# Performance work log

Hardware: AMD Instinct MI355X
Metric: run time of the kernel (lower is better)

The kernel has to match this reference:

```python
import jax, jax.numpy as jnp
import numpy as np

B, N, D, KD = 8, 2048, 64, 64

def setup_inputs() -> dict:
    key = jax.random.key(0)
    ks = jax.random.split(key, 7)
    s = 1.0 / np.sqrt(D)
    return {
        "x":  jax.random.normal(ks[0], (B, N, D), dtype=jnp.float32),
        "Wq": jax.random.normal(ks[1], (D, KD), dtype=jnp.float32) * s,
        "bq": jnp.zeros((KD,), jnp.float32),
        "Wk": jax.random.normal(ks[2], (D, KD), dtype=jnp.float32) * s,
        "bk": jnp.zeros((KD,), jnp.float32),
        "Wv": jax.random.normal(ks[3], (D, KD), dtype=jnp.float32) * s,
        "bv": jnp.zeros((KD,), jnp.float32),
    }

def reference(x, Wq, bq, Wk, bk, Wv, bv):
    # Q,K,V: [B,N,KD]
    Q = x @ Wq + bq
    K = x @ Wk + bk
    V = x @ Wv + bv
    # scores: [B,N,N] (note: original applies NO 1/sqrt(d) scaling)
    scores = jnp.einsum('bij,bkj->bik', Q, K)
    probs = jax.nn.softmax(scores, axis=-1)
    # mean-threshold sparsification: keep entries above the row mean
    mask = (probs > jnp.mean(probs, axis=-1, keepdims=True)).astype(probs.dtype)
    sparse = probs * mask
    out = jnp.einsum('bij,bjk->bik', sparse, V)  # [B,N,KD]
    return out
```

## Files before the change

kernel.cpp:

```cpp
#include <hip/hip_runtime.h>

#define NB 8
#define NS 2048
#define ND 64
#define LOG2E 1.44269504f

typedef _Float16 half8 __attribute__((ext_vector_type(8)));
typedef _Float16 half4 __attribute__((ext_vector_type(4)));
typedef __attribute__((ext_vector_type(4))) float floatx4;

__device__ __forceinline__ half8 cvt8(const float* p) {
    float4 a = *(const float4*)p;
    float4 b = *(const float4*)(p + 4);
    half8 h = {(_Float16)a.x, (_Float16)a.y, (_Float16)a.z, (_Float16)a.w,
               (_Float16)b.x, (_Float16)b.y, (_Float16)b.z, (_Float16)b.w};
    return h;
}

__global__ __launch_bounds__(256) void wprep(
    const float* __restrict__ Wq, const float* __restrict__ Wk,
    const float* __restrict__ Wv, _Float16* __restrict__ Wt)
{
    const int m = blockIdx.x;
    const float* W = (m == 0) ? Wq : (m == 1) ? Wk : Wv;
    for (int i = threadIdx.x; i < 64 * 64; i += 256) {
        const int c = i >> 6, d = i & 63;
        Wt[((size_t)m * 64 + c) * 64 + d] = (_Float16)W[d * 64 + c];
    }
}

__global__ __launch_bounds__(256) void qkv_proj(
    const float* __restrict__ x, const _Float16* __restrict__ Wt,
    const float* __restrict__ bq, const float* __restrict__ bk,
    const float* __restrict__ bv,
    _Float16* __restrict__ Qg, _Float16* __restrict__ Kg,
    _Float16* __restrict__ Vt)
{
    __shared__ _Float16 vt[4][64 * 20];

    const int tid  = threadIdx.x;
    const int wv   = tid >> 6;
    const int l    = tid & 63;
    const int quad = l >> 4;
    const int tx   = l & 15;

    const int b  = blockIdx.x & 7;
    const int n0 = (blockIdx.x >> 3) * 64 + wv * 16;

    const float* xr = x + ((size_t)b * NS + n0 + tx) * ND + quad * 8;
    half8 a0 = cvt8(xr);
    half8 a1 = cvt8(xr + 32);

    const floatx4 zf = {0.f, 0.f, 0.f, 0.f};

#pragma unroll
    for (int ctile = 0; ctile < 12; ++ctile) {
        const int m    = ctile >> 2;
        const int lcol = (ctile & 3) * 16 + tx;

        const _Float16* Wb = Wt + ((size_t)m * 64 + lcol) * 64;
        half8 b0 = *(const half8*)(Wb + quad * 8);
        half8 b1 = *(const half8*)(Wb + 32 + quad * 8);

        floatx4 acc = __builtin_amdgcn_mfma_f32_16x16x32_f16(a0, b0, zf, 0, 0, 0);
        acc = __builtin_amdgcn_mfma_f32_16x16x32_f16(a1, b1, acc, 0, 0, 0);

        const float* Bp = (m == 0) ? bq : (m == 1) ? bk : bv;
        const float bias = Bp[lcol];

        if (m == 0) {
#pragma unroll
            for (int r = 0; r < 4; ++r)
                Qg[((size_t)b * NS + n0 + quad * 4 + r) * ND + lcol] =
                    (_Float16)((acc[r] + bias) * LOG2E);
        } else if (m == 1) {
#pragma unroll
            for (int r = 0; r < 4; ++r)
                Kg[((size_t)b * NS + n0 + quad * 4 + r) * ND + lcol] =
                    (_Float16)(acc[r] + bias);
        } else {
#pragma unroll
            for (int r = 0; r < 4; ++r)
                vt[wv][lcol * 20 + quad * 4 + r] = (_Float16)(acc[r] + bias);
        }
    }
    __syncthreads();
    {
        const int d = l;
        const _Float16* src = &vt[wv][d * 20];
        uint2 p0 = *(const uint2*)(src);
        uint2 p1 = *(const uint2*)(src + 4);
        uint2 p2 = *(const uint2*)(src + 8);
        uint2 p3 = *(const uint2*)(src + 12);
        uint4 q0 = {p0.x, p0.y, p1.x, p1.y};
        uint4 q1 = {p2.x, p2.y, p3.x, p3.y};
        _Float16* dst = Vt + ((size_t)b * ND + d) * NS + n0;
        *(uint4*)(dst)     = q0;
        *(uint4*)(dst + 8) = q1;
    }
}

__global__ __launch_bounds__(512, 2) void attn(
    const _Float16* __restrict__ Qg,
    const _Float16* __restrict__ Kg,
    const _Float16* __restrict__ Vt,
    float* __restrict__ out)
{
    __shared__ __align__(16) _Float16 smem[2 * 64 * 72 + 2 * 64 * 72];
    __shared__ float lsh[4 * 32];

    _Float16* ksm = smem;
    _Float16* vsm = smem + 2 * 64 * 72;

    const int tid  = threadIdx.x;
    const int wv   = tid >> 6;
    const int l    = tid & 63;
    const int quad = l >> 4;
    const int tx   = l & 15;
    const int rh   = wv >> 2;
    const int kq   = wv & 3;

    const int b  = blockIdx.x & 7;
    const int q0 = (blockIdx.x >> 3) * 32;

    const _Float16* Qb = Qg + ((size_t)b * NS + q0 + rh * 16) * ND;
    const _Float16* Kb = Kg + (size_t)b * NS * ND;
    const _Float16* Vb = Vt + (size_t)b * ND * NS;

    half8 qf[2];
#pragma unroll
    for (int kc = 0; kc < 2; ++kc)
        qf[kc] = *(const half8*)(Qb + (size_t)tx * ND + kc * 32 + quad * 8);

    const int skey = tid >> 3;
    const int sc   = tid & 7;
    const _Float16* Ksrc = Kb + (size_t)skey * ND + sc * 8;
    const _Float16* Vsrc = Vb + (size_t)skey * NS + sc * 8;
    const int sdst = skey * 72 + ((sc ^ (skey & 7)) * 8);

    const floatx4 zf = {0.f, 0.f, 0.f, 0.f};
    const int t7    = tx & 7;
    const int krow  = (kq * 16 + tx) * 72;
    const int koff0 = (quad ^ t7) * 8;
    const int koff1 = ((quad ^ 4) ^ t7) * 8;

    float lacc = 0.f;
    {
        uint4 gk = *(const uint4*)Ksrc;
        *(uint4*)(ksm + sdst) = gk;
        for (int t = 0; t < 32; ++t) {
            const int buf = (t & 1) * 4608;
            __syncthreads();
            if (t < 31) gk = *(const uint4*)(Ksrc + (size_t)(t + 1) * 64 * ND);
            half8 kf0 = *(const half8*)(ksm + buf + krow + koff0);
            half8 kf1 = *(const half8*)(ksm + buf + krow + koff1);
            floatx4 c = __builtin_amdgcn_mfma_f32_16x16x32_f16(kf0, qf[0], zf, 0, 0, 0);
            c = __builtin_amdgcn_mfma_f32_16x16x32_f16(kf1, qf[1], c, 0, 0, 0);
            lacc += __builtin_amdgcn_exp2f(c[0]) + __builtin_amdgcn_exp2f(c[1])
                  + __builtin_amdgcn_exp2f(c[2]) + __builtin_amdgcn_exp2f(c[3]);
            if (t < 31) *(uint4*)(ksm + (buf ^ 4608) + sdst) = gk;
        }
    }
#pragma unroll
    for (int off = 16; off < 64; off <<= 1)
        lacc += __shfl_xor(lacc, off);
    if (quad == 0)
        lsh[kq * 32 + rh * 16 + tx] = lacc;

    uint4 gk = *(const uint4*)Ksrc;
    uint4 gv = *(const uint4*)Vsrc;
    __syncthreads();

    float thr, inv;
    {
        const int row = rh * 16 + tx;
        float L = lsh[row] + lsh[32 + row] + lsh[64 + row] + lsh[96 + row];
        inv = 1.f / L;
        thr = L * (1.f / (float)NS);
    }

    *(uint4*)(ksm + sdst) = gk;
    *(uint4*)(vsm + sdst) = gv;

    const int vchunk = ((kq * 2 + (quad >> 1)) ^ t7) * 8 + (quad & 1) * 4;

    floatx4 o[4] = {zf, zf, zf, zf};

    for (int t = 0; t < 32; ++t) {
        const int buf = (t & 1) * 4608;
        __syncthreads();
        if (t < 31) {
            gk = *(const uint4*)(Ksrc + (size_t)(t + 1) * 64 * ND);
            gv = *(const uint4*)(Vsrc + (size_t)(t + 1) * 64);
        }
        half8 kf0 = *(const half8*)(ksm + buf + krow + koff0);
        half8 kf1 = *(const half8*)(ksm + buf + krow + koff1);
        half4 vf[4];
#pragma unroll
        for (int dg = 0; dg < 4; ++dg)
            vf[dg] = *(const half4*)(vsm + buf + (dg * 16 + tx) * 72 + vchunk);

        floatx4 c = __builtin_amdgcn_mfma_f32_16x16x32_f16(kf0, qf[0], zf, 0, 0, 0);
        c = __builtin_amdgcn_mfma_f32_16x16x32_f16(kf1, qf[1], c, 0, 0, 0);
        float e0 = __builtin_amdgcn_exp2f(c[0]);
        float e1 = __builtin_amdgcn_exp2f(c[1]);
        float e2 = __builtin_amdgcn_exp2f(c[2]);
        float e3 = __builtin_amdgcn_exp2f(c[3]);
        float w0 = (e0 > thr) ? e0 * inv : 0.f;
        float w1 = (e1 > thr) ? e1 * inv : 0.f;
        float w2 = (e2 > thr) ? e2 * inv : 0.f;
        float w3 = (e3 > thr) ? e3 * inv : 0.f;
        half4 af = {(_Float16)w0, (_Float16)w1, (_Float16)w2, (_Float16)w3};
#pragma unroll
        for (int dg = 0; dg < 4; ++dg)
            o[dg] = __builtin_amdgcn_mfma_f32_16x16x16f16(af, vf[dg], o[dg], 0, 0, 0);

        if (t < 31) {
            *(uint4*)(ksm + (buf ^ 4608) + sdst) = gk;
            *(uint4*)(vsm + (buf ^ 4608) + sdst) = gv;
        }
    }

    __syncthreads();
    float* osm = (float*)smem;
    const int orow = rh * 16 + quad * 4;
    if (kq == 0) {
#pragma unroll
        for (int dg = 0; dg < 4; ++dg)
#pragma unroll
            for (int r = 0; r < 4; ++r)
                osm[(orow + r) * 68 + dg * 16 + tx] = o[dg][r];
    }
    __syncthreads();
    if (kq == 1) {
#pragma unroll
        for (int dg = 0; dg < 4; ++dg)
#pragma unroll
            for (int r = 0; r < 4; ++r)
                osm[(orow + r) * 68 + dg * 16 + tx] += o[dg][r];
    }
    __syncthreads();
    if (kq == 2) {
#pragma unroll
        for (int dg = 0; dg < 4; ++dg)
#pragma unroll
            for (int r = 0; r < 4; ++r)
                osm[(orow + r) * 68 + dg * 16 + tx] += o[dg][r];
    }
    __syncthreads();
    if (kq == 3) {
#pragma unroll
        for (int dg = 0; dg < 4; ++dg)
#pragma unroll
            for (int r = 0; r < 4; ++r)
                out[((size_t)b * NS + q0 + orow + r) * ND + dg * 16 + tx] =
                    osm[(orow + r) * 68 + dg * 16 + tx] + o[dg][r];
    }
}

extern "C" void kernel_launch(void* const* d_in, const int* in_sizes, int n_in,
                              void* d_out, int out_size, void* d_ws, size_t ws_size,
                              hipStream_t stream) {
    const float* x  = (const float*)d_in[0];
    const float* Wq = (const float*)d_in[1];
    const float* bq = (const float*)d_in[2];
    const float* Wk = (const float*)d_in[3];
    const float* bk = (const float*)d_in[4];
    const float* Wv = (const float*)d_in[5];
    const float* bv = (const float*)d_in[6];

    _Float16* Qg = (_Float16*)d_ws;
    _Float16* Kg = Qg + (size_t)NB * NS * ND;
    _Float16* Vt = Kg + (size_t)NB * NS * ND;
    _Float16* Wt = Vt + (size_t)NB * NS * ND;

    wprep<<<3, 256, 0, stream>>>(Wq, Wk, Wv, Wt);
    qkv_proj<<<NB * (NS / 64), 256, 0, stream>>>(x, Wt, bq, bk, bv, Qg, Kg, Vt);
    attn<<<NB * (NS / 32), 512, 0, stream>>>(Qg, Kg, Vt, (float*)d_out);
}
```

Before: 113.5 us.

## Cache quantized scores in registers to skip recomputing QK^T in second pass

The first pass now computes scores over 128-key tiles, quantizes each score to a 16-bit fixed-point value (scale 256), and keeps all of them packed in registers. The second pass streams only V and rebuilds the weights from the cached scores, so K is not reloaded and the QK MFMAs are not run twice. Tiles grow to 128 keys, swizzling is replaced by padded strides, and the occupancy hint moves to 4 blocks. This adds register pressure and introduces quantization error plus clamping of large scores, which can change which entries pass the mean threshold.

```diff
diff --git a/kernel.cpp b/kernel.cpp
--- a/kernel.cpp
+++ b/kernel.cpp
@@ -4,6 +4,13 @@
 #define NS 2048
 #define ND 64
 #define LOG2E 1.44269504f
+#define QSC 256.0f
+#define IQS (1.0f / 256.0f)
+
+#define KST 80
+#define VST 136
+#define KTILE (128 * KST)
+#define VTILE (64 * VST)
 
 typedef _Float16 half8 __attribute__((ext_vector_type(8)));
 typedef _Float16 half4 __attribute__((ext_vector_type(4)));
@@ -100,17 +107,14 @@
     }
 }
 
-__global__ __launch_bounds__(512, 2) void attn(
+__global__ __launch_bounds__(512, 4) void attn(
     const _Float16* __restrict__ Qg,
     const _Float16* __restrict__ Kg,
     const _Float16* __restrict__ Vt,
     float* __restrict__ out)
 {
-    __shared__ __align__(16) _Float16 smem[2 * 64 * 72 + 2 * 64 * 72];
+    __shared__ __align__(16) _Float16 smem[2 * KTILE];
     __shared__ float lsh[4 * 32];
-
-    _Float16* ksm = smem;
-    _Float16* vsm = smem + 2 * 64 * 72;
 
     const int tid  = threadIdx.x;
     const int wv   = tid >> 6;
@@ -132,33 +136,52 @@
     for (int kc = 0; kc < 2; ++kc)
         qf[kc] = *(const half8*)(Qb + (size_t)tx * ND + kc * 32 + quad * 8);
 
-    const int skey = tid >> 3;
-    const int sc   = tid & 7;
-    const _Float16* Ksrc = Kb + (size_t)skey * ND + sc * 8;
-    const _Float16* Vsrc = Vb + (size_t)skey * NS + sc * 8;
-    const int sdst = skey * 72 + ((sc ^ (skey & 7)) * 8);
-
     const floatx4 zf = {0.f, 0.f, 0.f, 0.f};
-    const int t7    = tx & 7;
-    const int krow  = (kq * 16 + tx) * 72;
-    const int koff0 = (quad ^ t7) * 8;
-    const int koff1 = ((quad ^ 4) ^ t7) * 8;
+
+    uint2 sr[32];
 
     float lacc = 0.f;
     {
-        uint4 gk = *(const uint4*)Ksrc;
-        *(uint4*)(ksm + sdst) = gk;
-        for (int t = 0; t < 32; ++t) {
-            const int buf = (t & 1) * 4608;
+        const int skey = tid >> 2;
+        const int sc0  = tid & 3;
+        const _Float16* Ksrc = Kb + (size_t)skey * ND + sc0 * 8;
+        const int kd = skey * KST + sc0 * 8;
+
+        uint4 ga = *(const uint4*)Ksrc;
+        uint4 gb = *(const uint4*)(Ksrc + 32);
+        *(uint4*)(smem + kd) = ga;
+        *(uint4*)(smem + kd + 32) = gb;
+
+#pragma unroll
+        for (int t = 0; t < 16; ++t) {
+            const int buf = (t & 1) * KTILE;
             __syncthreads();
-            if (t < 31) gk = *(const uint4*)(Ksrc + (size_t)(t + 1) * 64 * ND);
-            half8 kf0 = *(const half8*)(ksm + buf + krow + koff0);
-            half8 kf1 = *(const half8*)(ksm + buf + krow + koff1);
-            floatx4 c = __builtin_amdgcn_mfma_f32_16x16x32_f16(kf0, qf[0], zf, 0, 0, 0);
-            c = __builtin_amdgcn_mfma_f32_16x16x32_f16(kf1, qf[1], c, 0, 0, 0);
-            lacc += __builtin_amdgcn_exp2f(c[0]) + __builtin_amdgcn_exp2f(c[1])
-                  + __builtin_amdgcn_exp2f(c[2]) + __builtin_amdgcn_exp2f(c[3]);
-            if (t < 31) *(uint4*)(ksm + (buf ^ 4608) + sdst) = gk;
+            if (t < 15) {
+                ga = *(const uint4*)(Ksrc + (size_t)(t + 1) * 128 * ND);
+                gb = *(const uint4*)(Ksrc + (size_t)(t + 1) * 128 * ND + 32);
+            }
+#pragma unroll
+            for (int g = 0; g < 2; ++g) {
+                const int krow = buf + (kq * 32 + g * 16 + tx) * KST;
+                half8 kf0 = *(const half8*)(smem + krow + quad * 8);
+                half8 kf1 = *(const half8*)(smem + krow + 32 + quad * 8);
+                floatx4 c = __builtin_amdgcn_mfma_f32_16x16x32_f16(kf0, qf[0], zf, 0, 0, 0);
+                c = __builtin_amdgcn_mfma_f32_16x16x32_f16(kf1, qf[1], c, 0, 0, 0);
+                int ic[4];
+#pragma unroll
+                for (int r = 0; r < 4; ++r) {
+                    float cs = fminf(fmaxf(c[r] * QSC, -32000.f), 32000.f);
+                    int v = (int)rintf(cs);
+                    ic[r] = v;
+                    lacc += __builtin_amdgcn_exp2f((float)v * IQS);
+                }
+                sr[t * 2 + g].x = (unsigned)(ic[0] & 0xffff) | ((unsigned)ic[1] << 16);
+                sr[t * 2 + g].y = (unsigned)(ic[2] & 0xffff) | ((unsigned)ic[3] << 16);
+            }
+            if (t < 15) {
+                *(uint4*)(smem + (buf ^ KTILE) + kd) = ga;
+                *(uint4*)(smem + (buf ^ KTILE) + kd + 32) = gb;
+            }
         }
     }
 #pragma unroll
@@ -167,8 +190,13 @@
     if (quad == 0)
         lsh[kq * 32 + rh * 16 + tx] = lacc;
 
-    uint4 gk = *(const uint4*)Ksrc;
-    uint4 gv = *(const uint4*)Vsrc;
+    const int sdim = tid >> 3;
+    const int sv0  = tid & 7;
+    const _Float16* Vsrc = Vb + (size_t)sdim * NS + sv0 * 8;
+    const int vd = sdim * VST + sv0 * 8;
+
+    uint4 gva = *(const uint4*)Vsrc;
+    uint4 gvb = *(const uint4*)(Vsrc + 64);
     __syncthreads();
 
     float thr, inv;
@@ -179,45 +207,43 @@
         thr = L * (1.f / (float)NS);
     }
 
-    *(uint4*)(ksm + sdst) = gk;
-    *(uint4*)(vsm + sdst) = gv;
-
-    const int vchunk = ((kq * 2 + (quad >> 1)) ^ t7) * 8 + (quad & 1) * 4;
+    *(uint4*)(smem + vd) = gva;
+    *(uint4*)(smem + vd + 64) = gvb;
 
     floatx4 o[4] = {zf, zf, zf, zf};
 
-    for (int t = 0; t < 32; ++t) {
-        const int buf = (t & 1) * 4608;
+#pragma unroll
+    for (int t = 0; t < 16; ++t) {
+        const int buf = (t & 1) * VTILE;
         __syncthreads();
-        if (t < 31) {
-            gk = *(const uint4*)(Ksrc + (size_t)(t + 1) * 64 * ND);
-            gv = *(const uint4*)(Vsrc + (size_t)(t + 1) * 64);
-        }
-        half8 kf0 = *(const half8*)(ksm + buf + krow + koff0);
-        half8 kf1 = *(const half8*)(ksm + buf + krow + koff1);
-        half4 vf[4];
-#pragma unroll
-        for (int dg = 0; dg < 4; ++dg)
-            vf[dg] = *(const half4*)(vsm + buf + (dg * 16 + tx) * 72 + vchunk);
-
-        floatx4 c = __builtin_amdgcn_mfma_f32_16x16x32_f16(kf0, qf[0], zf, 0, 0, 0);
-        c = __builtin_amdgcn_mfma_f32_16x16x32_f16(kf1, qf[1], c, 0, 0, 0);
-        float e0 = __builtin_amdgcn_exp2f(c[0]);
-        float e1 = __builtin_amdgcn_exp2f(c[1]);
-        float e2 = __builtin_amdgcn_exp2f(c[2]);
-        float e3 = __builtin_amdgcn_exp2f(c[3]);
-        float w0 = (e0 > thr) ? e0 * inv : 0.f;
-        float w1 = (e1 > thr) ? e1 * inv : 0.f;
-        float w2 = (e2 > thr) ? e2 * inv : 0.f;
-        float w3 = (e3 > thr) ? e3 * inv : 0.f;
-        half4 af = {(_Float16)w0, (_Float16)w1, (_Float16)w2, (_Float16)w3};
-#pragma unroll
-        for (int dg = 0; dg < 4; ++dg)
-            o[dg] = __builtin_amdgcn_mfma_f32_16x16x16f16(af, vf[dg], o[dg], 0, 0, 0);
-
-        if (t < 31) {
-            *(uint4*)(ksm + (buf ^ 4608) + sdst) = gk;
-            *(uint4*)(vsm + (buf ^ 4608) + sdst) = gv;
+        if (t < 15) {
+            gva = *(const uint4*)(Vsrc + (size_t)(t + 1) * 128);
+            gvb = *(const uint4*)(Vsrc + (size_t)(t + 1) * 128 + 64);
+        }
+#pragma unroll
+        for (int g = 0; g < 2; ++g) {
+            const uint2 u = sr[t * 2 + g];
+            int s0 = (int)(short)(u.x), s1 = (int)(short)(u.x >> 16);
+            int s2 = (int)(short)(u.y), s3 = (int)(short)(u.y >> 16);
+            float e0 = __builtin_amdgcn_exp2f((float)s0 * IQS);
+            float e1 = __builtin_amdgcn_exp2f((float)s1 * IQS);
+            float e2 = __builtin_amdgcn_exp2f((float)s2 * IQS);
+            float e3 = __builtin_amdgcn_exp2f((float)s3 * IQS);
+            float w0 = (e0 > thr) ? e0 * inv : 0.f;
+            float w1 = (e1 > thr) ? e1 * inv : 0.f;
+            float w2 = (e2 > thr) ? e2 * inv : 0.f;
+            float w3 = (e3 > thr) ? e3 * inv : 0.f;
+            half4 af = {(_Float16)w0, (_Float16)w1, (_Float16)w2, (_Float16)w3};
+#pragma unroll
+            for (int dg = 0; dg < 4; ++dg) {
+                half4 vf = *(const half4*)(smem + buf + (dg * 16 + tx) * VST +
+                                           kq * 32 + g * 16 + quad * 4);
+                o[dg] = __builtin_amdgcn_mfma_f32_16x16x16f16(af, vf, o[dg], 0, 0, 0);
+            }
+        }
+        if (t < 15) {
+            *(uint4*)(smem + (buf ^ VTILE) + vd) = gva;
+            *(uint4*)(smem + (buf ^ VTILE) + vd + 64) = gvb;
         }
     }
 
```

Measured after the change: 132.6 us. +16.9%, slower.
